# Kernel optimization log

Hardware: AMD Instinct MI355X
Metric: run time of the kernel (lower is better)

The kernel has to match this reference:

```python
import jax, jax.numpy as jnp
import numpy as np

EMBED_DIM = 768
HEAD_SIZE = 64

def setup_inputs() -> dict:
    key = jax.random.key(0)
    k1, k2, k3, k4 = jax.random.split(key, 4)
    x = jax.random.normal(k1, (4, 4096, EMBED_DIM), dtype=jnp.float32)
    # nn.Linear(E, H, bias=False) weights, stored as [E, H] for y = x @ W
    scale = 1.0 / np.sqrt(EMBED_DIM)
    Wk = jax.random.uniform(k2, (EMBED_DIM, HEAD_SIZE), jnp.float32, -scale, scale)
    Wq = jax.random.uniform(k3, (EMBED_DIM, HEAD_SIZE), jnp.float32, -scale, scale)
    Wv = jax.random.uniform(k4, (EMBED_DIM, HEAD_SIZE), jnp.float32, -scale, scale)
    return {"x": x, "Wk": Wk, "Wq": Wq, "Wv": Wv}

def reference(x, Wk, Wq, Wv):
    # x: [B, S, E]
    E = x.shape[2]
    K = jnp.einsum("bse,eh->bsh", x, Wk)  # [B, S, H]
    Q = jnp.einsum("bse,eh->bsh", x, Wq)
    V = jnp.einsum("bse,eh->bsh", x, Wv)
    # NOTE: original scales by embedding_dim**0.5, not head_size**0.5
    A = jnp.einsum("bqh,bkh->bqk", Q, K) / jnp.sqrt(jnp.asarray(E, x.dtype))
    A = jax.nn.softmax(A, axis=-1)
    # dropout is inference-mode identity
    return jnp.einsum("bqk,bkh->bqh", A, V)
```

## Files before the change

### kernel.cpp

```cpp
#include <hip/hip_runtime.h>

typedef __attribute__((ext_vector_type(8))) short short8;
typedef __attribute__((ext_vector_type(4))) short short4v;
typedef __attribute__((ext_vector_type(4))) float float4v;
typedef __attribute__((ext_vector_type(2))) int int2v;

__device__ __forceinline__ short f2bf(float f) {
    union { float f; unsigned u; } v; v.f = f;
    return (short)((v.u + 0x7fffu + ((v.u >> 16) & 1u)) >> 16);
}
__device__ __forceinline__ int pack2(float a, float b) {
    union { float f; unsigned u; } x, y; x.f = a; y.f = b;
    return (int)(((x.u + 0x8000u) >> 16) | ((y.u + 0x8000u) & 0xFFFF0000u));
}

__device__ __forceinline__ float fast_exp2(float x) {
#if __has_builtin(__builtin_amdgcn_exp2f)
    return __builtin_amdgcn_exp2f(x);
#else
    return exp2f(x);
#endif
}

__global__ void wtrans_kernel(const float* __restrict__ Wk, const float* __restrict__ Wq,
                              const float* __restrict__ Wv, short* __restrict__ Wt3T) {
    int idx = blockIdx.x * 256 + threadIdx.x;
    int p = idx / 12288;
    int rem = idx - p * 12288;
    int kstep = rem / 512;
    int r2 = rem - kstep * 512;
    int lane = r2 >> 3, i = r2 & 7;
    int quad = lane >> 4, l16 = lane & 15;
    int j = p >> 2, nt = p & 3;
    int n = nt * 16 + l16;
    int k = kstep * 32 + quad * 8 + i;
    const float* W = (j == 0) ? Wq : (j == 1 ? Wk : Wv);
    float scale = (j == 0) ? 0.05205877f : 1.0f;
    Wt3T[idx] = f2bf(W[k * 64 + n] * scale);
}

__global__ __launch_bounds__(256, 3) void proj_kernel(
    const float* __restrict__ x, const short* __restrict__ Wt3T,
    short* __restrict__ Qs, short* __restrict__ Kb, short* __restrict__ Vtr)
{
    __shared__ alignas(16) short As[24 * 512];
    const int tid = threadIdx.x;
    const int wave = tid >> 6, lane = tid & 63, quad = lane >> 4, l16 = lane & 15;
    const int m0 = blockIdx.x * 16;
    const int p0 = wave * 3;

    {
        const int r = tid >> 4, c16 = tid & 15;
        const float* xp = x + (size_t)(m0 + r) * 768 + c16 * 4;
        float4 v[12];
#pragma unroll
        for (int ch = 0; ch < 12; ++ch) v[ch] = *(const float4*)(xp + ch * 64);
#pragma unroll
        for (int ch = 0; ch < 12; ++ch) {
            const int cb = c16 * 4 + ch * 64;
            const int sidx = (cb >> 5) * 512 + ((((cb >> 3) & 3) * 16 + r) << 3) + (cb & 7);
            *(int2v*)&As[sidx] = (int2v){pack2(v[ch].x, v[ch].y), pack2(v[ch].z, v[ch].w)};
        }
    }
    __syncthreads();

    const short* wp0 = Wt3T + (size_t)(p0 + 0) * 12288 + lane * 8;
    const short* wp1 = Wt3T + (size_t)(p0 + 1) * 12288 + lane * 8;
    const short* wp2 = Wt3T + (size_t)(p0 + 2) * 12288 + lane * 8;

    float4v acc0 = (float4v){0.f, 0.f, 0.f, 0.f};
    float4v acc1 = acc0, acc2 = acc0;

#pragma unroll
    for (int it = 0; it < 24; ++it) {
        short8 a = *(const short8*)&As[it * 512 + lane * 8];
        short8 w0 = *(const short8*)(wp0 + it * 512);
        short8 w1 = *(const short8*)(wp1 + it * 512);
        short8 w2 = *(const short8*)(wp2 + it * 512);
        acc0 = __builtin_amdgcn_mfma_f32_16x16x32_bf16(a, w0, acc0, 0, 0, 0);
        acc1 = __builtin_amdgcn_mfma_f32_16x16x32_bf16(a, w1, acc1, 0, 0, 0);
        acc2 = __builtin_amdgcn_mfma_f32_16x16x32_bf16(a, w2, acc2, 0, 0, 0);
    }

    float4v accs[3] = {acc0, acc1, acc2};
#pragma unroll
    for (int t = 0; t < 3; ++t) {
        const int p = p0 + t, j = p >> 2, nt = p & 3;
        if (j < 2) {
            short* dst = (j == 0) ? Qs : Kb;
#pragma unroll
            for (int r = 0; r < 4; ++r)
                dst[(size_t)(m0 + quad * 4 + r) * 64 + nt * 16 + l16] = f2bf(accs[t][r]);
        }
    }
    __syncthreads();
    short* sm = As;
#pragma unroll
    for (int t = 0; t < 3; ++t) {
        const int p = p0 + t, nt = p & 3;
        if ((p >> 2) == 2)
#pragma unroll
            for (int r = 0; r < 4; ++r)
                sm[(quad * 4 + r) * 72 + nt * 16 + l16] = f2bf(accs[t][r]);
    }
    __syncthreads();
    {
        const int h = tid >> 2, si = (tid & 3) * 4;
        const int b = m0 >> 12, s0 = m0 & 4095;
        short4v tmp;
#pragma unroll
        for (int i = 0; i < 4; ++i) tmp[i] = sm[(si + i) * 72 + h];
        *(short4v*)(Vtr + (size_t)(b * 64 + h) * 4096 + s0 + si) = tmp;
    }
}

__global__ __launch_bounds__(256, 4) void attn_kernel(
    const short* __restrict__ Qs, const short* __restrict__ Kb, const short* __restrict__ Vt,
    float* __restrict__ out, float* __restrict__ Lsum, int kv_len)
{
    __shared__ alignas(16) short Kl[64 * 72];
    __shared__ alignas(16) short Vl[64 * 72];
    __shared__ alignas(16) short Pl[4 * 32 * 72];

    const int tid = threadIdx.x;
    const int wave = tid >> 6, lane = tid & 63, quad = lane >> 4, l16 = lane & 15;
    const int qt = blockIdx.x, b = blockIdx.y, sp = blockIdx.z;
    const int q0 = qt * 128;
    const int bS = b * 4096;
    const int kv0 = sp * kv_len;

    short8 qa[2][2];
#pragma unroll
    for (int qt2 = 0; qt2 < 2; ++qt2)
#pragma unroll
        for (int ks = 0; ks < 2; ++ks)
            qa[qt2][ks] = *(const short8*)(Qs + (size_t)(bS + q0 + wave * 32 + qt2 * 16 + l16) * 64 + ks * 32 + quad * 8);

    float4v o[2][4];
    float rs[2] = {0.f, 0.f};
#pragma unroll
    for (int qt2 = 0; qt2 < 2; ++qt2)
#pragma unroll
        for (int nt = 0; nt < 4; ++nt) o[qt2][nt] = (float4v){0.f, 0.f, 0.f, 0.f};

    const int sr = tid >> 2, sc = (tid & 3) * 16;
    short* plw = &Pl[wave * 2304];

    const short* kp = Kb + (size_t)(bS + kv0 + sr) * 64 + sc;
    const short* vp = Vt + (size_t)(b * 64 + sr) * 4096 + kv0 + sc;
    short8 kr0 = *(const short8*)kp,       kr1 = *(const short8*)(kp + 8);
    short8 vr0 = *(const short8*)vp,       vr1 = *(const short8*)(vp + 8);

    for (int kt = 0; kt < kv_len; kt += 64) {
        __syncthreads();
        *(short8*)&Kl[sr * 72 + sc]     = kr0;
        *(short8*)&Kl[sr * 72 + sc + 8] = kr1;
        *(short8*)&Vl[sr * 72 + sc]     = vr0;
        *(short8*)&Vl[sr * 72 + sc + 8] = vr1;
        __syncthreads();

        if (kt + 64 < kv_len) {
            kp += 64 * 64; vp += 64;
            kr0 = *(const short8*)kp; kr1 = *(const short8*)(kp + 8);
            vr0 = *(const short8*)vp; vr1 = *(const short8*)(vp + 8);
        }

#pragma unroll
        for (int kvt = 0; kvt < 4; ++kvt) {
            short8 ka0 = *(const short8*)&Kl[(kvt * 16 + l16) * 72 + quad * 8];
            short8 ka1 = *(const short8*)&Kl[(kvt * 16 + l16) * 72 + 32 + quad * 8];
#pragma unroll
            for (int qt2 = 0; qt2 < 2; ++qt2) {
                float4v a0 = (float4v){0.f, 0.f, 0.f, 0.f};
                a0 = __builtin_amdgcn_mfma_f32_16x16x32_bf16(ka0, qa[qt2][0], a0, 0, 0, 0);
                a0 = __builtin_amdgcn_mfma_f32_16x16x32_bf16(ka1, qa[qt2][1], a0, 0, 0, 0);
                float p0 = fast_exp2(a0[0]), p1 = fast_exp2(a0[1]);
                float p2 = fast_exp2(a0[2]), p3 = fast_exp2(a0[3]);
                rs[qt2] += (p0 + p1) + (p2 + p3);
                *(int2v*)&plw[(qt2 * 16 + l16) * 72 + kvt * 16 + quad * 4] =
                    (int2v){pack2(p0, p1), pack2(p2, p3)};
            }
        }

#pragma unroll
        for (int ks = 0; ks < 2; ++ks) {
            short8 bf[4];
#pragma unroll
            for (int nt = 0; nt < 4; ++nt)
                bf[nt] = *(const short8*)&Vl[(nt * 16 + l16) * 72 + ks * 32 + quad * 8];
#pragma unroll
            for (int qt2 = 0; qt2 < 2; ++qt2) {
                short8 af = *(const short8*)&plw[(qt2 * 16 + l16) * 72 + ks * 32 + quad * 8];
#pragma unroll
                for (int nt = 0; nt < 4; ++nt)
                    o[qt2][nt] = __builtin_amdgcn_mfma_f32_16x16x32_bf16(af, bf[nt], o[qt2][nt], 0, 0, 0);
            }
        }
    }

#pragma unroll
    for (int qt2 = 0; qt2 < 2; ++qt2) {
        rs[qt2] += __shfl_xor(rs[qt2], 16);
        rs[qt2] += __shfl_xor(rs[qt2], 32);
    }

#pragma unroll
    for (int qt2 = 0; qt2 < 2; ++qt2) {
#pragma unroll
        for (int nt = 0; nt < 4; ++nt)
#pragma unroll
            for (int r = 0; r < 4; ++r) {
                int qb = q0 + wave * 32 + qt2 * 16 + quad * 4 + r;
                atomicAdd(&out[(size_t)(bS + qb) * 64 + nt * 16 + l16], o[qt2][nt][r]);
            }
        if (quad == 0)
            atomicAdd(&Lsum[bS + q0 + wave * 32 + qt2 * 16 + l16], rs[qt2]);
    }
}

__global__ void normalize_kernel(float* __restrict__ out, const float* __restrict__ Lsum) {
    int idx = blockIdx.x * 256 + threadIdx.x;
    out[idx] /= Lsum[idx >> 6];
}

extern "C" void kernel_launch(void* const* d_in, const int* in_sizes, int n_in,
                              void* d_out, int out_size, void* d_ws, size_t ws_size,
                              hipStream_t stream) {
    const float* x  = (const float*)d_in[0];
    const float* Wk = (const float*)d_in[1];
    const float* Wq = (const float*)d_in[2];
    const float* Wv = (const float*)d_in[3];
    float* out = (float*)d_out;

    char* w = (char*)d_ws;
    size_t off = 0;
    auto take = [&](size_t bytes) -> void* {
        void* p = w + off;
        off = (off + bytes + 255) & ~(size_t)255;
        return p;
    };
    short* Qs   = (short*)take((size_t)16384 * 64 * 2);
    short* Kb   = (short*)take((size_t)16384 * 64 * 2);
    short* Vt   = (short*)take((size_t)16384 * 64 * 2);
    short* Wt3  = (short*)take((size_t)3 * 64 * 768 * 2);
    float* Lsum = (float*)take((size_t)16384 * 4);

    hipMemsetAsync(out, 0, (size_t)out_size * sizeof(float), stream);
    hipMemsetAsync(Lsum, 0, (size_t)16384 * 4, stream);

    wtrans_kernel<<<576, 256, 0, stream>>>(Wk, Wq, Wv, Wt3);
    proj_kernel<<<1024, 256, 0, stream>>>(x, Wt3, Qs, Kb, Vt);
    const int nsplit = 8;
    dim3 ag(32, 4, nsplit);
    attn_kernel<<<ag, 256, 0, stream>>>(Qs, Kb, Vt, out, Lsum, 4096 / nsplit);
    normalize_kernel<<<4096, 256, 0, stream>>>(out, Lsum);
}
```

Measured before the change: 146.2 us.

## Load K/V fragments directly from global memory, dropping LDS staging and block syncs

The attention kernel no longer stages K and V tiles through shared memory with two barriers per iteration. Each wave now reads its MFMA K and V operands straight from global memory (served by L1/L2) and keeps only a small per-wave P buffer in LDS. Blocks shrink to 128 threads (two waves, 64 queries) and the grid doubles to keep the same total work. This removes barriers and LDS traffic, but K/V reuse across waves now relies on caches and the explicit prefetch-ahead of the next tile is gone, so load latency may be exposed.

Result: slower. 188.2 us (+28.8%).

```diff
diff --git a/kernel.cpp b/kernel.cpp
--- a/kernel.cpp
+++ b/kernel.cpp
@@ -114,27 +114,25 @@
     }
 }
 
-__global__ __launch_bounds__(256, 4) void attn_kernel(
+__global__ __launch_bounds__(128, 4) void attn_kernel(
     const short* __restrict__ Qs, const short* __restrict__ Kb, const short* __restrict__ Vt,
     float* __restrict__ out, float* __restrict__ Lsum, int kv_len)
 {
-    __shared__ alignas(16) short Kl[64 * 72];
-    __shared__ alignas(16) short Vl[64 * 72];
-    __shared__ alignas(16) short Pl[4 * 32 * 72];
+    __shared__ alignas(16) short Pl[2][2][32 * 40];
 
     const int tid = threadIdx.x;
     const int wave = tid >> 6, lane = tid & 63, quad = lane >> 4, l16 = lane & 15;
     const int qt = blockIdx.x, b = blockIdx.y, sp = blockIdx.z;
-    const int q0 = qt * 128;
+    const int q0 = qt * 64 + wave * 32;
     const int bS = b * 4096;
     const int kv0 = sp * kv_len;
 
-    short8 qa[2][2];
+    short8 qb[2][2];
 #pragma unroll
     for (int qt2 = 0; qt2 < 2; ++qt2)
 #pragma unroll
         for (int ks = 0; ks < 2; ++ks)
-            qa[qt2][ks] = *(const short8*)(Qs + (size_t)(bS + q0 + wave * 32 + qt2 * 16 + l16) * 64 + ks * 32 + quad * 8);
+            qb[qt2][ks] = *(const short8*)(Qs + (size_t)(bS + q0 + qt2 * 16 + l16) * 64 + ks * 32 + quad * 8);
 
     float4v o[2][4];
     float rs[2] = {0.f, 0.f};
@@ -143,54 +141,38 @@
 #pragma unroll
         for (int nt = 0; nt < 4; ++nt) o[qt2][nt] = (float4v){0.f, 0.f, 0.f, 0.f};
 
-    const int sr = tid >> 2, sc = (tid & 3) * 16;
-    short* plw = &Pl[wave * 2304];
-
-    const short* kp = Kb + (size_t)(bS + kv0 + sr) * 64 + sc;
-    const short* vp = Vt + (size_t)(b * 64 + sr) * 4096 + kv0 + sc;
-    short8 kr0 = *(const short8*)kp,       kr1 = *(const short8*)(kp + 8);
-    short8 vr0 = *(const short8*)vp,       vr1 = *(const short8*)(vp + 8);
+    const short* kbase = Kb + (size_t)bS * 64;
+    const short* vbase = Vt + (size_t)b * 64 * 4096;
 
     for (int kt = 0; kt < kv_len; kt += 64) {
-        __syncthreads();
-        *(short8*)&Kl[sr * 72 + sc]     = kr0;
-        *(short8*)&Kl[sr * 72 + sc + 8] = kr1;
-        *(short8*)&Vl[sr * 72 + sc]     = vr0;
-        *(short8*)&Vl[sr * 72 + sc + 8] = vr1;
-        __syncthreads();
-
-        if (kt + 64 < kv_len) {
-            kp += 64 * 64; vp += 64;
-            kr0 = *(const short8*)kp; kr1 = *(const short8*)(kp + 8);
-            vr0 = *(const short8*)vp; vr1 = *(const short8*)(vp + 8);
-        }
-
-#pragma unroll
-        for (int kvt = 0; kvt < 4; ++kvt) {
-            short8 ka0 = *(const short8*)&Kl[(kvt * 16 + l16) * 72 + quad * 8];
-            short8 ka1 = *(const short8*)&Kl[(kvt * 16 + l16) * 72 + 32 + quad * 8];
+        const int kvg = kv0 + kt;
+#pragma unroll
+        for (int hf = 0; hf < 2; ++hf) {
+            short* plh = &Pl[wave][hf][0];
+#pragma unroll
+            for (int kvt2 = 0; kvt2 < 2; ++kvt2) {
+                const short* krow = kbase + (size_t)(kvg + hf * 32 + kvt2 * 16 + l16) * 64 + quad * 8;
+                short8 ka0 = *(const short8*)krow;
+                short8 ka1 = *(const short8*)(krow + 32);
+#pragma unroll
+                for (int qt2 = 0; qt2 < 2; ++qt2) {
+                    float4v a0 = (float4v){0.f, 0.f, 0.f, 0.f};
+                    a0 = __builtin_amdgcn_mfma_f32_16x16x32_bf16(ka0, qb[qt2][0], a0, 0, 0, 0);
+                    a0 = __builtin_amdgcn_mfma_f32_16x16x32_bf16(ka1, qb[qt2][1], a0, 0, 0, 0);
+                    float p0 = fast_exp2(a0[0]), p1 = fast_exp2(a0[1]);
+                    float p2 = fast_exp2(a0[2]), p3 = fast_exp2(a0[3]);
+                    rs[qt2] += (p0 + p1) + (p2 + p3);
+                    *(int2v*)&plh[(qt2 * 16 + l16) * 40 + kvt2 * 16 + quad * 4] =
+                        (int2v){pack2(p0, p1), pack2(p2, p3)};
+                }
+            }
+            short8 bf[4];
+#pragma unroll
+            for (int nt = 0; nt < 4; ++nt)
+                bf[nt] = *(const short8*)(vbase + (size_t)(nt * 16 + l16) * 4096 + kvg + hf * 32 + quad * 8);
 #pragma unroll
             for (int qt2 = 0; qt2 < 2; ++qt2) {
-                float4v a0 = (float4v){0.f, 0.f, 0.f, 0.f};
-                a0 = __builtin_amdgcn_mfma_f32_16x16x32_bf16(ka0, qa[qt2][0], a0, 0, 0, 0);
-                a0 = __builtin_amdgcn_mfma_f32_16x16x32_bf16(ka1, qa[qt2][1], a0, 0, 0, 0);
-                float p0 = fast_exp2(a0[0]), p1 = fast_exp2(a0[1]);
-                float p2 = fast_exp2(a0[2]), p3 = fast_exp2(a0[3]);
-                rs[qt2] += (p0 + p1) + (p2 + p3);
-                *(int2v*)&plw[(qt2 * 16 + l16) * 72 + kvt * 16 + quad * 4] =
-                    (int2v){pack2(p0, p1), pack2(p2, p3)};
-            }
-        }
-
-#pragma unroll
-        for (int ks = 0; ks < 2; ++ks) {
-            short8 bf[4];
-#pragma unroll
-            for (int nt = 0; nt < 4; ++nt)
-                bf[nt] = *(const short8*)&Vl[(nt * 16 + l16) * 72 + ks * 32 + quad * 8];
-#pragma unroll
-            for (int qt2 = 0; qt2 < 2; ++qt2) {
-                short8 af = *(const short8*)&plw[(qt2 * 16 + l16) * 72 + ks * 32 + quad * 8];
+                short8 af = *(const short8*)&plh[(qt2 * 16 + l16) * 40 + quad * 8];
 #pragma unroll
                 for (int nt = 0; nt < 4; ++nt)
                     o[qt2][nt] = __builtin_amdgcn_mfma_f32_16x16x32_bf16(af, bf[nt], o[qt2][nt], 0, 0, 0);
@@ -210,11 +192,11 @@
         for (int nt = 0; nt < 4; ++nt)
 #pragma unroll
             for (int r = 0; r < 4; ++r) {
-                int qb = q0 + wave * 32 + qt2 * 16 + quad * 4 + r;
-                atomicAdd(&out[(size_t)(bS + qb) * 64 + nt * 16 + l16], o[qt2][nt][r]);
+                int qb2 = q0 + qt2 * 16 + quad * 4 + r;
+                atomicAdd(&out[(size_t)(bS + qb2) * 64 + nt * 16 + l16], o[qt2][nt][r]);
             }
         if (quad == 0)
-            atomicAdd(&Lsum[bS + q0 + wave * 32 + qt2 * 16 + l16], rs[qt2]);
+            atomicAdd(&Lsum[bS + q0 + qt2 * 16 + l16], rs[qt2]);
     }
 }
 
@@ -251,7 +233,7 @@
     wtrans_kernel<<<576, 256, 0, stream>>>(Wk, Wq, Wv, Wt3);
     proj_kernel<<<1024, 256, 0, stream>>>(x, Wt3, Qs, Kb, Vt);
     const int nsplit = 8;
-    dim3 ag(32, 4, nsplit);
-    attn_kernel<<<ag, 256, 0, stream>>>(Qs, Kb, Vt, out, Lsum, 4096 / nsplit);
+    dim3 ag(64, 4, nsplit);
+    attn_kernel<<<ag, 128, 0, stream>>>(Qs, Kb, Vt, out, Lsum, 4096 / nsplit);
     normalize_kernel<<<4096, 256, 0, stream>>>(out, Lsum);
 }
```
